# Kernel tuning notes

Hardware: AMD Instinct MI355X
Metric: run time of the kernel (lower is better)

Reference implementation:

```python
import jax, jax.numpy as jnp
import numpy as np

N_T, N_M, E, Q = 100000, 20000, 600000, 200000
F_IN, D, L = 256, 128, 2


def setup_inputs() -> dict:
    key = jax.random.key(0)
    ks = jax.random.split(key, 20)
    s = 1.0 / np.sqrt(D)
    inp = {
        "x_thesis": jax.random.normal(ks[0], (N_T, F_IN), jnp.float32),
        "mentor_node_id": jnp.arange(N_M, dtype=jnp.int64) if jax.config.jax_enable_x64 else jnp.arange(N_M, dtype=jnp.int32),
        "edge_src": jax.random.randint(ks[1], (E,), 0, N_T),
        "edge_dst": jax.random.randint(ks[2], (E,), 0, N_M),
        "eli_src": jax.random.randint(ks[3], (Q,), 0, N_T),
        "eli_dst": jax.random.randint(ks[4], (Q,), 0, N_M),
        # encoder params
        "thesis_lin_w": jax.random.normal(ks[5], (D, F_IN), jnp.float32) / np.sqrt(F_IN),
        "thesis_lin_b": jnp.zeros((D,), jnp.float32),
        "prof_emb": jax.random.normal(ks[6], (N_M, D), jnp.float32),
        # SAGEConv params per layer, per edge type (sup: thesis->mentor, rev: mentor->thesis)
        "W_nbr_sup": jax.random.normal(ks[7], (L, D, D), jnp.float32) * s,
        "W_root_sup": jax.random.normal(ks[8], (L, D, D), jnp.float32) * s,
        "b_sup": jnp.zeros((L, D), jnp.float32),
        "W_nbr_rev": jax.random.normal(ks[9], (L, D, D), jnp.float32) * s,
        "W_root_rev": jax.random.normal(ks[10], (L, D, D), jnp.float32) * s,
        "b_rev": jnp.zeros((L, D), jnp.float32),
        # classifier Linear(2*D -> 1)
        "cls_w": jax.random.normal(ks[11], (2 * D,), jnp.float32) * (1.0 / np.sqrt(2 * D)),
        "cls_b": jnp.zeros((), jnp.float32),
    }
    return inp


def reference(x_thesis, mentor_node_id, edge_src, edge_dst, eli_src, eli_dst,
              thesis_lin_w, thesis_lin_b, prof_emb,
              W_nbr_sup, W_root_sup, b_sup, W_nbr_rev, W_root_rev, b_rev,
              cls_w, cls_b):
    n_t = x_thesis.shape[0]
    n_m = prof_emb.shape[0]
    L_ = W_nbr_sup.shape[0]

    # node encoders
    h_t = x_thesis @ thesis_lin_w.T + thesis_lin_b          # [N_T, D]
    h_m = prof_emb[mentor_node_id]                          # [N_M, D]

    ones = jnp.ones(edge_src.shape[0], h_t.dtype)
    deg_m = jnp.maximum(jax.ops.segment_sum(ones, edge_dst, num_segments=n_m), 1.0)[:, None]
    deg_t = jnp.maximum(jax.ops.segment_sum(ones, edge_src, num_segments=n_t), 1.0)[:, None]

    for l in range(L_):
        # mean-aggregate thesis feats onto mentors (supervised_by edges)
        agg_m = jax.ops.segment_sum(h_t[edge_src], edge_dst, num_segments=n_m) / deg_m
        # mean-aggregate mentor feats onto theses (reverse edges)
        agg_t = jax.ops.segment_sum(h_m[edge_dst], edge_src, num_segments=n_t) / deg_t
        new_m = agg_m @ W_nbr_sup[l].T + h_m @ W_root_sup[l].T + b_sup[l]
        new_t = agg_t @ W_nbr_rev[l].T + h_t @ W_root_rev[l].T + b_rev[l]
        if l < L_ - 1:
            new_m = jax.nn.relu(new_m)
            new_t = jax.nn.relu(new_t)
        h_t, h_m = new_t, new_m

    # edge-level classifier: gather endpoints, concat, linear -> scalar per pair
    z = jnp.concatenate([h_t[eli_src], h_m[eli_dst]], axis=-1)  # [Q, 2D]
    return z @ cls_w + cls_b                                     # [Q]
```

## Files before the change

### kernel.cpp

```cpp
#include <hip/hip_runtime.h>
#include <cstdint>
#include <cstddef>

#define D 128
#define F_IN 256

typedef __attribute__((ext_vector_type(8))) short bf16x8;
typedef __attribute__((ext_vector_type(4))) float f32x4;

__device__ __forceinline__ unsigned short f2bs(float f) {
  unsigned int x = __builtin_bit_cast(unsigned int, f);
  x = x + 0x7fffu + ((x >> 16) & 1u);
  return (unsigned short)(x >> 16);
}
__device__ __forceinline__ unsigned pk2(float lo, float hi) {
  return (unsigned)f2bs(lo) | ((unsigned)f2bs(hi) << 16);
}
__device__ __forceinline__ float b2f(unsigned int lo16) {
  unsigned int x = lo16 << 16;
  return __builtin_bit_cast(float, x);
}
__device__ __forceinline__ void gl_lds16v(const void* g, void* l) {
  __builtin_amdgcn_global_load_lds(
      (__attribute__((address_space(1))) void*)g,
      (__attribute__((address_space(3))) void*)l, 16, 0, 0);
}
__device__ __forceinline__ uint4 pack8(float4 a, float4 b) {
  uint4 o;
  o.x = pk2(a.x, a.y); o.y = pk2(a.z, a.w);
  o.z = pk2(b.x, b.y); o.w = pk2(b.z, b.w);
  return o;
}


__global__ __launch_bounds__(256) void prep_k(
    const float* __restrict__ s0, unsigned short* __restrict__ d0, int n0,
    const float* __restrict__ s1, unsigned short* __restrict__ d1, int n1,
    const float* __restrict__ s2, unsigned short* __restrict__ d2, int n2,
    const float* __restrict__ s3, unsigned short* __restrict__ d3, int n3,
    const float* __restrict__ s4, unsigned short* __restrict__ d4, int n4,
    int nbC,
    const float* __restrict__ emb, const int* __restrict__ ids,
    unsigned short* __restrict__ hm, int NM, int nbG,
    const int* __restrict__ esrc, const int* __restrict__ edst,
    int* __restrict__ bktT, int* __restrict__ bktM,
    int E, int SHT, int SHM, int nbA)
{
  int bid = blockIdx.x;
  int tid = threadIdx.x;
  if (bid < nbC) {
    int j = bid * 256 + tid;
    const float* s; unsigned short* d;
    if (j < n0) { s = s0; d = d0; }
    else {
      j -= n0;
      if (j < n1) { s = s1; d = d1; }
      else {
        j -= n1;
        if (j < n2) { s = s2; d = d2; }
        else {
          j -= n2;
          if (j < n3) { s = s3; d = d3; }
          else { j -= n3; if (j >= n4) return; s = s4; d = d4; }
        }
      }
    }
    const float4* sp = (const float4*)(s + (size_t)j * 8);
    *(uint4*)(d + (size_t)j * 8) = pack8(sp[0], sp[1]);
    return;
  }
  bid -= nbC;
  if (bid < nbG) {
    int i = bid * 256 + tid;
    if (i >= NM * 16) return;
    int r = i >> 4, c = (i & 15) * 8;
    const float* s = emb + (size_t)ids[r] * D + c;
    *(uint4*)(hm + (size_t)r * D + c) = pack8(*(const float4*)s, *(const float4*)(s + 4));
    return;
  }
  bid -= nbG;
  __shared__ int sh[256];
  sh[tid] = 0;
  __syncthreads();
  int stride = nbA * 256;
  for (int e = bid * 256 + tid; e < E; e += stride) {
    atomicAdd(&sh[esrc[e] >> SHT], 1);
    atomicAdd(&sh[128 + (edst[e] >> SHM)], 1);
  }
  __syncthreads();
  if (tid < 128) { if (sh[tid]) atomicAdd(&bktT[tid], sh[tid]); }
  else { if (sh[tid]) atomicAdd(&bktM[tid - 128], sh[tid]); }
}


__global__ void a2_scan_k(const int* __restrict__ bktT, int* __restrict__ baseT, int* __restrict__ curT, int BT,
                          const int* __restrict__ bktM, int* __restrict__ baseM, int* __restrict__ curM, int BM) {
  __shared__ int sT[129], sM[129];
  int tid = threadIdx.x;
  if (tid < BT) sT[tid] = bktT[tid];
  if (tid < BM) sM[tid] = bktM[tid];
  __syncthreads();
  if (tid == 0) { int r = 0; for (int i = 0; i < BT; ++i) { int c = sT[i]; sT[i] = r; r += c; } sT[BT] = r; }
  if (tid == 1) { int r = 0; for (int i = 0; i < BM; ++i) { int c = sM[i]; sM[i] = r; r += c; } sM[BM] = r; }
  __syncthreads();
  if (tid <= BT) { baseT[tid] = sT[tid]; if (tid < BT) curT[tid] = sT[tid]; }
  if (tid <= BM) { baseM[tid] = sM[tid]; if (tid < BM) curM[tid] = sM[tid]; }
}


#define CH 4096

__device__ __forceinline__ void a3_body(
    const int* __restrict__ esrc, const int* __restrict__ edst,
    unsigned* __restrict__ partT, unsigned* __restrict__ partM,
    int* __restrict__ curT, int* __restrict__ curM,
    int E, int BT, int BM, int SHT, int SHM, int blk, char* smraw)
{
  unsigned* stT = (unsigned*)smraw;
  unsigned* stM = stT + CH;
  int* hT  = (int*)(stM + CH);
  int* lbT = hT + 128;
  int* lcT = hT + 256;
  int* gbT = hT + 384;
  int* hM  = hT + 512;
  int* lbM = hT + 640;
  int* lcM = hT + 768;
  int* gbM = hT + 896;
  int* st2 = hT + 1024;

  int tid = threadIdx.x;
  int c0 = blk * CH;
  int len = E - c0; if (len > CH) len = CH;

  if (tid < 128) { hT[tid] = 0; hM[tid] = 0; }
  __syncthreads();
  for (int i = tid; i < len; i += 256) {
    atomicAdd(&hT[esrc[c0 + i] >> SHT], 1);
    atomicAdd(&hM[edst[c0 + i] >> SHM], 1);
  }
  __syncthreads();
  int own = (tid < 128) ? hT[tid] : hM[tid - 128];
  st2[tid] = own;
  __syncthreads();
  for (int dd = 1; dd < 128; dd <<= 1) {
    int y = ((tid & 127) >= dd) ? st2[tid - dd] : 0;
    __syncthreads();
    st2[tid] += y;
    __syncthreads();
  }
  int excl = st2[tid] - own;
  if (tid < 128) { lbT[tid] = excl; lcT[tid] = excl; }
  else { lbM[tid - 128] = excl; lcM[tid - 128] = excl; }
  __syncthreads();
  if (tid < BT) { if (hT[tid]) gbT[tid] = atomicAdd(&curT[tid], hT[tid]); }
  if (tid >= 128 && tid - 128 < BM) { int m = tid - 128; if (hM[m]) gbM[m] = atomicAdd(&curM[m], hM[m]); }
  __syncthreads();
  for (int i = tid; i < len; i += 256) {
    unsigned s = (unsigned)esrc[c0 + i], dn = (unsigned)edst[c0 + i];
    int p = atomicAdd(&lcT[s >> SHT], 1);
    stT[p] = (s << 15) | dn;
    int q = atomicAdd(&lcM[dn >> SHM], 1);
    stM[q] = (dn << 17) | s;
  }
  __syncthreads();
  for (int b = 0; b < BT; ++b) {
    int cb = hT[b]; if (!cb) continue;
    int lb = lbT[b]; int gb = gbT[b];
    for (int i = tid; i < cb; i += 256) partT[gb + i] = stT[lb + i];
  }
  for (int b = 0; b < BM; ++b) {
    int cb = hM[b]; if (!cb) continue;
    int lb = lbM[b]; int gb = gbM[b];
    for (int i = tid; i < cb; i += 256) partM[gb + i] = stM[lb + i];
  }
}


__device__ __forceinline__ void enc_body(
    const float* __restrict__ A, const unsigned short* __restrict__ W,
    const float* __restrict__ bias, unsigned short* __restrict__ out, int M,
    int blk, char* smraw)
{
  float* bufA0 = (float*)smraw;
  unsigned short* bufW0 = (unsigned short*)(smraw + 32768);
  const int tid = threadIdx.x;
  const int w = tid >> 6, l = tid & 63;
  const int wr = w >> 1, wc = w & 1;
  const int lr = l & 15, kg = l >> 4;
  const int row0 = blk * 128;
  const int arow = l >> 3;
  const int au = l & 7;
  const int wrow = l >> 2;
  const int wu = l & 3;

  f32x4 acc[4][4] = {};

  auto stage = [&](int st, int bsel) {
    int k0 = st * 32;
    float* bA = bufA0 + bsel * 4096;
    unsigned short* bW = bufW0 + bsel * 4096;
#pragma unroll
    for (int q = 0; q < 4; ++q) {
      int r = w * 32 + q * 8 + arow;
      int gr = row0 + r; if (gr >= M) gr = M - 1;
      int gu = au ^ (r & 7);
      gl_lds16v(A + (size_t)gr * F_IN + k0 + gu * 4, bA + (w * 32 + q * 8) * 32 + l * 4);
    }
#pragma unroll
    for (int q = 0; q < 2; ++q) {
      int r = w * 32 + q * 16 + wrow;
      int gu = wu ^ ((r >> 1) & 3);
      gl_lds16v(W + (size_t)r * F_IN + k0 + gu * 8, bW + (w * 32 + q * 16) * 32 + l * 8);
    }
  };

  stage(0, 0);
#pragma unroll 1
  for (int st = 0; st < F_IN / 32; ++st) {
    if (st < F_IN / 32 - 1) {
      stage(st + 1, (st + 1) & 1);
      __builtin_amdgcn_sched_barrier(0);
      asm volatile("s_waitcnt vmcnt(6)" ::: "memory");
    } else {
      __builtin_amdgcn_sched_barrier(0);
      asm volatile("s_waitcnt vmcnt(0)" ::: "memory");
    }
    __builtin_amdgcn_s_barrier();
    __builtin_amdgcn_sched_barrier(0);
    const float* bA = bufA0 + (st & 1) * 4096;
    const unsigned short* bW = bufW0 + (st & 1) * 4096;
    bf16x8 aF[4], bF[4];
#pragma unroll
    for (int i = 0; i < 4; ++i) {
      int r = wr * 64 + i * 16 + lr;
      const float4* pa = (const float4*)(bA + r * 32);
      float4 v0 = pa[(2 * kg) ^ (r & 7)];
      float4 v1 = pa[(2 * kg + 1) ^ (r & 7)];
      uint4 c = pack8(v0, v1);
      aF[i] = *(bf16x8*)&c;
    }
#pragma unroll
    for (int j = 0; j < 4; ++j) {
      int r = wc * 64 + j * 16 + lr;
      bF[j] = *(const bf16x8*)&bW[r * 32 + ((kg ^ ((r >> 1) & 3)) * 8)];
    }
#pragma unroll
    for (int i = 0; i < 4; ++i)
#pragma unroll
      for (int j = 0; j < 4; ++j)
        acc[i][j] = __builtin_amdgcn_mfma_f32_16x16x32_bf16(aF[i], bF[j], acc[i][j], 0, 0, 0);
    __builtin_amdgcn_sched_barrier(0);
    __builtin_amdgcn_s_barrier();
  }

  __syncthreads();
  float bn[4];
#pragma unroll
  for (int j = 0; j < 4; ++j) bn[j] = bias[wc * 64 + j * 16 + lr];
  unsigned short* ow = (unsigned short*)smraw + w * 4096;
#pragma unroll
  for (int i = 0; i < 4; ++i)
#pragma unroll
    for (int j = 0; j < 4; ++j) {
      f32x4 v = acc[i][j];
#pragma unroll
      for (int r = 0; r < 4; ++r)
        ow[(i * 16 + kg * 4 + r) * 64 + j * 16 + lr] = f2bs(v[r] + bn[j]);
    }
  __syncthreads();
#pragma unroll
  for (int q = 0; q < 8; ++q) {
    int u = q * 64 + l;
    int lrow = u >> 3;
    int cu = (u & 7) * 8;
    int gr = row0 + wr * 64 + lrow;
    if (gr < M)
      *(uint4*)(out + (size_t)gr * D + wc * 64 + cu) = *(const uint4*)&ow[lrow * 64 + cu];
  }
}

__global__ __launch_bounds__(256) void a3enc_k(
    const int* __restrict__ esrc, const int* __restrict__ edst,
    unsigned* __restrict__ partT, unsigned* __restrict__ partM,
    int* __restrict__ curT, int* __restrict__ curM,
    int E, int BT, int BM, int SHT, int SHM, int nbA3,
    const float* __restrict__ A, const unsigned short* __restrict__ W,
    const float* __restrict__ bias, unsigned short* __restrict__ out, int M)
{
  __shared__ char smraw[49152];
  if ((int)blockIdx.x < nbA3)
    a3_body(esrc, edst, partT, partM, curT, curM, E, BT, BM, SHT, SHM, blockIdx.x, smraw);
  else
    enc_body(A, W, bias, out, M, blockIdx.x - nbA3, smraw);
}


#define BCAP 12288

__global__ __launch_bounds__(256) void b_csr_k(
    const unsigned* __restrict__ partT, const int* __restrict__ baseT,
    int* __restrict__ rowT, int* __restrict__ csrT, int NT, int BT, int SHT,
    const unsigned* __restrict__ partM, const int* __restrict__ baseM,
    int* __restrict__ rowM, int* __restrict__ csrM, int NM, int BM, int SHM, int E)
{
  __shared__ int cnt[1024];
  __shared__ int st[256];
  __shared__ unsigned stage[BCAP];

  const unsigned* part; const int* base; int* row; int* csr;
  int N, SH, KS; unsigned PM; int b; bool last;
  if ((int)blockIdx.x < BT) {
    part = partT; base = baseT; row = rowT; csr = csrT;
    N = NT; SH = SHT; KS = 15; PM = 0x7fffu; b = blockIdx.x; last = (b == BT - 1);
  } else {
    part = partM; base = baseM; row = rowM; csr = csrM;
    N = NM; SH = SHM; KS = 17; PM = 0x1ffffu; b = blockIdx.x - BT; last = (b == BM - 1);
  }
  int tid = threadIdx.x;
  int ebeg = base[b], eend = base[b + 1];
  int tot = eend - ebeg;
  int n0 = b << SH;
  int width = 1 << SH;
  int nw = N - n0; if (nw > width) nw = width;
  int seg = (width + 255) >> 8;

  for (int j = 0; j < seg; ++j) { int idx = tid * seg + j; if (idx < nw) cnt[idx] = 0; }
  __syncthreads();
  for (int i = tid; i < tot; i += 256) {
    int k = (int)(part[ebeg + i] >> KS) - n0;
    atomicAdd(&cnt[k], 1);
  }
  __syncthreads();
  int s = 0;
  for (int j = 0; j < seg; ++j) { int idx = tid * seg + j; if (idx < nw) s += cnt[idx]; }
  st[tid] = s;
  __syncthreads();
  for (int dd = 1; dd < 256; dd <<= 1) {
    int y = (tid >= dd) ? st[tid - dd] : 0;
    __syncthreads();
    st[tid] += y;
    __syncthreads();
  }
  int run = st[tid] - s;
  for (int j = 0; j < seg; ++j) {
    int idx = tid * seg + j;
    if (idx < nw) {
      int c = cnt[idx];
      row[n0 + idx] = ebeg + run;
      cnt[idx] = run;
      run += c;
    }
  }
  if (last && tid == 0) row[N] = E;
  __syncthreads();
  if (tot <= BCAP) {
    for (int i = tid; i < tot; i += 256) {
      unsigned p = part[ebeg + i];
      int k = (int)(p >> KS) - n0;
      int pos = atomicAdd(&cnt[k], 1);
      stage[pos] = p & PM;
    }
    __syncthreads();
    for (int i = tid; i < tot; i += 256) csr[ebeg + i] = (int)stage[i];
  } else {
    for (int i = tid; i < tot; i += 256) {
      unsigned p = part[ebeg + i];
      int k = (int)(p >> KS) - n0;
      int pos = atomicAdd(&cnt[k], 1);
      csr[ebeg + pos] = (int)(p & PM);
    }
  }
}


__global__ __launch_bounds__(256) void aggregate3_k(
    const unsigned short* __restrict__ tabM, const int* __restrict__ rowpM,
    const int* __restrict__ idxM, unsigned short* __restrict__ outM, int nM, int nblkM,
    const unsigned short* __restrict__ tabT, const int* __restrict__ rowpT,
    const int* __restrict__ idxT, unsigned short* __restrict__ outT, int nT)
{
  const unsigned short* tab; const int* rowp; const int* idx;
  unsigned short* outp; int n, nodeb;
  if ((int)blockIdx.x < nblkM) {
    tab = tabM; rowp = rowpM; idx = idxM; outp = outM; n = nM;
    nodeb = blockIdx.x * 8;
  } else {
    tab = tabT; rowp = rowpT; idx = idxT; outp = outT; n = nT;
    nodeb = (blockIdx.x - nblkM) * 8;
  }
  const int tid = threadIdx.x;
  const int l = tid & 63;
  const int sub = l >> 5;
  const int half = (l >> 4) & 1;
  const int l16 = l & 15;
  const int node = nodeb + (tid >> 6) * 2 + sub;
  const int nodeC = node < n ? node : n - 1;
  int b = rowp[nodeC];
  int e = rowp[nodeC + 1];
  if (node >= n) e = b;
  const int deg = e - b;
  int nb = (deg + 15) >> 4;
  int onb = __shfl_xor(nb, 32, 64);
  int trip = nb > onb ? nb : onb;
  const unsigned short* tl = tab + l16 * 8;

  float a0 = 0.f, a1 = 0.f, a2 = 0.f, a3 = 0.f;
  float a4 = 0.f, a5 = 0.f, a6 = 0.f, a7 = 0.f;
  for (int t = 0; t < trip; ++t) {
    int base = b + t * 16 + half;
    int pp[8]; bool ok[8];
#pragma unroll
    for (int u = 0; u < 8; ++u) {
      int p = base + 2 * u;
      ok[u] = p < e;
      pp[u] = ok[u] ? idx[p] : 0;
    }
    uint4 vv[8];
#pragma unroll
    for (int u = 0; u < 8; ++u) {
      uint4 z; z.x = 0u; z.y = 0u; z.z = 0u; z.w = 0u;
      vv[u] = z;
      if (ok[u]) vv[u] = *(const uint4*)(tl + (size_t)pp[u] * D);
    }
#pragma unroll
    for (int u = 0; u < 8; ++u) {
      a0 += b2f(vv[u].x & 0xffffu); a1 += b2f(vv[u].x >> 16);
      a2 += b2f(vv[u].y & 0xffffu); a3 += b2f(vv[u].y >> 16);
      a4 += b2f(vv[u].z & 0xffffu); a5 += b2f(vv[u].z >> 16);
      a6 += b2f(vv[u].w & 0xffffu); a7 += b2f(vv[u].w >> 16);
    }
  }
  a0 += __shfl_xor(a0, 16, 64);
  a1 += __shfl_xor(a1, 16, 64);
  a2 += __shfl_xor(a2, 16, 64);
  a3 += __shfl_xor(a3, 16, 64);
  a4 += __shfl_xor(a4, 16, 64);
  a5 += __shfl_xor(a5, 16, 64);
  a6 += __shfl_xor(a6, 16, 64);
  a7 += __shfl_xor(a7, 16, 64);
  if (node < n && half == 0) {
    float inv = 1.0f / (float)(deg > 1 ? deg : 1);
    uint4 o;
    o.x = pk2(a0 * inv, a1 * inv);
    o.y = pk2(a2 * inv, a3 * inv);
    o.z = pk2(a4 * inv, a5 * inv);
    o.w = pk2(a6 * inv, a7 * inv);
    *(uint4*)(outp + (size_t)node * D + l16 * 8) = o;
  }
}


template<bool RELU>
__device__ __forceinline__ void gemm_body(
    const unsigned short* __restrict__ Aop, const unsigned short* __restrict__ WA,
    const unsigned short* __restrict__ Bop, const unsigned short* __restrict__ WB,
    const float* __restrict__ bias, unsigned short* __restrict__ out, int M,
    int blk, char* smraw)
{
  unsigned short* bufA0 = (unsigned short*)smraw;
  unsigned short* bufW0 = (unsigned short*)(smraw + 16384);
  const int tid = threadIdx.x;
  const int w = tid >> 6, l = tid & 63;
  const int wr = w >> 1, wc = w & 1;
  const int lr = l & 15, kg = l >> 4;
  const int row0 = blk * 128;
  const int srow = l >> 2;
  const int su = l & 3;

  f32x4 acc[4][4] = {};

  auto stage = [&](int st, int bsel) {
    const unsigned short* Ap = (st < 4) ? Aop : Bop;
    const unsigned short* Wp = (st < 4) ? WA : WB;
    int k0 = (st & 3) * 32;
    unsigned short* bA = bufA0 + bsel * 4096;
    unsigned short* bW = bufW0 + bsel * 4096;
#pragma unroll
    for (int q = 0; q < 2; ++q) {
      int r = w * 32 + q * 16 + srow;
      int gr = row0 + r; if (gr >= M) gr = M - 1;
      int gu = su ^ ((r >> 1) & 3);
      gl_lds16v(Ap + (size_t)gr * D + k0 + gu * 8, bA + (w * 32 + q * 16) * 32 + l * 8);
      gl_lds16v(Wp + (size_t)r * D + k0 + gu * 8, bW + (w * 32 + q * 16) * 32 + l * 8);
    }
  };

  stage(0, 0);
#pragma unroll 1
  for (int st = 0; st < 8; ++st) {
    if (st < 7) {
      stage(st + 1, (st + 1) & 1);
      __builtin_amdgcn_sched_barrier(0);
      asm volatile("s_waitcnt vmcnt(4)" ::: "memory");
    } else {
      __builtin_amdgcn_sched_barrier(0);
      asm volatile("s_waitcnt vmcnt(0)" ::: "memory");
    }
    __builtin_amdgcn_s_barrier();
    __builtin_amdgcn_sched_barrier(0);
    const unsigned short* bA = bufA0 + (st & 1) * 4096;
    const unsigned short* bW = bufW0 + (st & 1) * 4096;
    bf16x8 aF[4], bF[4];
#pragma unroll
    for (int i = 0; i < 4; ++i) {
      int r = wr * 64 + i * 16 + lr;
      aF[i] = *(const bf16x8*)&bA[r * 32 + ((kg ^ ((r >> 1) & 3)) * 8)];
    }
#pragma unroll
    for (int j = 0; j < 4; ++j) {
      int r = wc * 64 + j * 16 + lr;
      bF[j] = *(const bf16x8*)&bW[r * 32 + ((kg ^ ((r >> 1) & 3)) * 8)];
    }
#pragma unroll
    for (int i = 0; i < 4; ++i)
#pragma unroll
      for (int j = 0; j < 4; ++j)
        acc[i][j] = __builtin_amdgcn_mfma_f32_16x16x32_bf16(aF[i], bF[j], acc[i][j], 0, 0, 0);
    __builtin_amdgcn_sched_barrier(0);
    __builtin_amdgcn_s_barrier();
  }

  __syncthreads();
  float bn[4];
#pragma unroll
  for (int j = 0; j < 4; ++j) bn[j] = bias[wc * 64 + j * 16 + lr];
  unsigned short* ow = (unsigned short*)smraw + w * 4096;
#pragma unroll
  for (int i = 0; i < 4; ++i)
#pragma unroll
    for (int j = 0; j < 4; ++j) {
      f32x4 v = acc[i][j];
#pragma unroll
      for (int r = 0; r < 4; ++r) {
        float x = v[r] + bn[j];
        if (RELU) x = fmaxf(x, 0.f);
        ow[(i * 16 + kg * 4 + r) * 64 + j * 16 + lr] = f2bs(x);
      }
    }
  __syncthreads();
#pragma unroll
  for (int q = 0; q < 8; ++q) {
    int u = q * 64 + l;
    int lrow = u >> 3;
    int cu = (u & 7) * 8;
    int gr = row0 + wr * 64 + lrow;
    if (gr < M)
      *(uint4*)(out + (size_t)gr * D + wc * 64 + cu) = *(const uint4*)&ow[lrow * 64 + cu];
  }
}

template<bool RELU>
__global__ __launch_bounds__(256) void gemm_pair_k(
    const unsigned short* __restrict__ Am, const unsigned short* __restrict__ WAm,
    const unsigned short* __restrict__ Bm, const unsigned short* __restrict__ WBm,
    const float* __restrict__ biasm, unsigned short* __restrict__ outm, int Mm, int nbm,
    const unsigned short* __restrict__ At, const unsigned short* __restrict__ WAt,
    const unsigned short* __restrict__ Bt, const unsigned short* __restrict__ WBt,
    const float* __restrict__ biast, unsigned short* __restrict__ outt, int Mt)
{
  __shared__ char smraw[32768];
  if ((int)blockIdx.x < nbm)
    gemm_body<RELU>(Am, WAm, Bm, WBm, biasm, outm, Mm, blockIdx.x, smraw);
  else
    gemm_body<RELU>(At, WAt, Bt, WBt, biast, outt, Mt, blockIdx.x - nbm, smraw);
}


__global__ __launch_bounds__(256) void classify_k(
    const unsigned short* __restrict__ ht, const unsigned short* __restrict__ hm,
    const int* __restrict__ qs, const int* __restrict__ qd,
    const float* __restrict__ w, const float* __restrict__ bptr,
    float* __restrict__ out, int Q)
{
  int g = blockIdx.x * 8 + (threadIdx.x >> 5);
  if (g >= Q) return;
  int l = threadIdx.x & 31;
  const unsigned short* src = (l < 16)
      ? ht + (size_t)qs[g] * D + l * 8
      : hm + (size_t)qd[g] * D + (l - 16) * 8;
  uint4 v = *(const uint4*)src;
  const float* wp = w + l * 8;
  float acc = 0.f;
  acc += b2f(v.x & 0xffffu) * wp[0];
  acc += b2f(v.x >> 16)     * wp[1];
  acc += b2f(v.y & 0xffffu) * wp[2];
  acc += b2f(v.y >> 16)     * wp[3];
  acc += b2f(v.z & 0xffffu) * wp[4];
  acc += b2f(v.z >> 16)     * wp[5];
  acc += b2f(v.w & 0xffffu) * wp[6];
  acc += b2f(v.w >> 16)     * wp[7];
#pragma unroll
  for (int m = 16; m >= 1; m >>= 1) acc += __shfl_xor(acc, m, 64);
  if (l == 0) out[g] = acc + bptr[0];
}


extern "C" void kernel_launch(void* const* d_in, const int* in_sizes, int n_in,
                              void* d_out, int out_size, void* d_ws, size_t ws_size,
                              hipStream_t stream)
{
  const float* x_thesis = (const float*)d_in[0];
  const int*   mentor_id = (const int*)d_in[1];
  const int*   esrc = (const int*)d_in[2];
  const int*   edst = (const int*)d_in[3];
  const int*   qsrc = (const int*)d_in[4];
  const int*   qdst = (const int*)d_in[5];
  const float* lin_w = (const float*)d_in[6];
  const float* lin_b = (const float*)d_in[7];
  const float* prof  = (const float*)d_in[8];
  const float* Wn_sup = (const float*)d_in[9];
  const float* Wr_sup = (const float*)d_in[10];
  const float* b_sup  = (const float*)d_in[11];
  const float* Wn_rev = (const float*)d_in[12];
  const float* Wr_rev = (const float*)d_in[13];
  const float* b_rev  = (const float*)d_in[14];
  const float* cls_w  = (const float*)d_in[15];
  const float* cls_b  = (const float*)d_in[16];

  const int NT = in_sizes[0] / F_IN;
  const int NM = in_sizes[1];
  const int E  = in_sizes[2];
  const int Q  = in_sizes[4];
  const int L  = in_sizes[11] / D;

  int SHT = 0; while ((((NT - 1) >> SHT) + 1) > 128) ++SHT;
  int SHM = 0; while ((((NM - 1) >> SHM) + 1) > 128) ++SHM;
  const int BT = ((NT - 1) >> SHT) + 1;
  const int BM = ((NM - 1) >> SHM) + 1;

  char* wsb = (char*)d_ws;
  size_t off = 0;
  auto alloc = [&](size_t bytes) {
    void* p = wsb + off;
    off = (off + bytes + 255) & ~(size_t)255;
    return p;
  };
  unsigned short* h_t   = (unsigned short*)alloc((size_t)NT * D * 2);
  unsigned short* a_t   = (unsigned short*)alloc((size_t)NT * D * 2);
  unsigned short* h_m   = (unsigned short*)alloc((size_t)NM * D * 2);
  unsigned short* a_m   = (unsigned short*)alloc((size_t)NM * D * 2);
  unsigned short* linw_bf = (unsigned short*)alloc((size_t)D * F_IN * 2);
  unsigned short* wns_bf  = (unsigned short*)alloc((size_t)L * D * D * 2);
  unsigned short* wrs_bf  = (unsigned short*)alloc((size_t)L * D * D * 2);
  unsigned short* wnr_bf  = (unsigned short*)alloc((size_t)L * D * D * 2);
  unsigned short* wrr_bf  = (unsigned short*)alloc((size_t)L * D * D * 2);
  int* row_t = (int*)alloc(((size_t)NT + 1) * 4);
  int* row_m = (int*)alloc(((size_t)NM + 1) * 4);
  int* csr_t = (int*)alloc((size_t)E * 4);
  int* csr_m = (int*)alloc((size_t)E * 4);
  unsigned* partT = (unsigned*)alloc((size_t)E * 4);
  unsigned* partM = (unsigned*)alloc((size_t)E * 4);
  size_t bkt_off = off;
  int* bktT  = (int*)alloc(128 * 4);
  int* bktM  = (int*)alloc(128 * 4);
  size_t bkt_end = off;
  int* baseT = (int*)alloc(129 * 4);
  int* baseM = (int*)alloc(129 * 4);
  int* curT  = (int*)alloc(128 * 4);
  int* curM  = (int*)alloc(128 * 4);
  (void)n_in; (void)out_size; (void)ws_size;

  (void)hipMemsetAsync(wsb + bkt_off, 0, bkt_end - bkt_off, stream);

  {
    int n0 = D * F_IN / 8, nw = L * D * D / 8;
    int totc = n0 + 4 * nw;
    int nbC = (totc + 255) / 256;
    int nbG = (NM * 16 + 255) / 256;
    int nbA = 256;
    prep_k<<<nbC + nbG + nbA, 256, 0, stream>>>(
        lin_w, linw_bf, n0, Wn_sup, wns_bf, nw, Wr_sup, wrs_bf, nw,
        Wn_rev, wnr_bf, nw, Wr_rev, wrr_bf, nw, nbC,
        prof, mentor_id, h_m, NM, nbG,
        esrc, edst, bktT, bktM, E, SHT, SHM, nbA);
  }
  a2_scan_k<<<1, 256, 0, stream>>>(bktT, baseT, curT, BT, bktM, baseM, curM, BM);

  int nbA3 = (E + CH - 1) / CH;
  int nbEnc = (NT + 127) / 128;
  a3enc_k<<<nbA3 + nbEnc, 256, 0, stream>>>(
      esrc, edst, partT, partM, curT, curM, E, BT, BM, SHT, SHM, nbA3,
      x_thesis, linw_bf, lin_b, h_t, NT);

  b_csr_k<<<BT + BM, 256, 0, stream>>>(
      partT, baseT, row_t, csr_t, NT, BT, SHT,
      partM, baseM, row_m, csr_m, NM, BM, SHM, E);

  int agg_nbm = (NM + 7) / 8, agg_nbt = (NT + 7) / 8;
  int gem_nbm = (NM + 127) / 128, gem_nbt = (NT + 127) / 128;
  for (int l = 0; l < L; ++l) {
    aggregate3_k<<<agg_nbm + agg_nbt, 256, 0, stream>>>(
        h_t, row_m, csr_m, a_m, NM, agg_nbm,
        h_m, row_t, csr_t, a_t, NT);

    const unsigned short* wns = wns_bf + (size_t)l * D * D;
    const unsigned short* wrs = wrs_bf + (size_t)l * D * D;
    const unsigned short* wnr = wnr_bf + (size_t)l * D * D;
    const unsigned short* wrr = wrr_bf + (size_t)l * D * D;
    const float* bs = b_sup + (size_t)l * D;
    const float* br = b_rev + (size_t)l * D;
    if (l < L - 1) {
      gemm_pair_k<true><<<gem_nbm + gem_nbt, 256, 0, stream>>>(
          a_m, wns, h_m, wrs, bs, a_m, NM, gem_nbm,
          a_t, wnr, h_t, wrr, br, a_t, NT);
    } else {
      gemm_pair_k<false><<<gem_nbm + gem_nbt, 256, 0, stream>>>(
          a_m, wns, h_m, wrs, bs, a_m, NM, gem_nbm,
          a_t, wnr, h_t, wrr, br, a_t, NT);
    }
    unsigned short* tmp;
    tmp = h_t; h_t = a_t; a_t = tmp;
    tmp = h_m; h_m = a_m; a_m = tmp;
  }

  classify_k<<<(Q + 7) / 8, 256, 0, stream>>>(h_t, h_m, qsrc, qdst, cls_w, cls_b,
                                              (float*)d_out, Q);
}
```

Before: 256.8 us.

## Move thesis encoder into prep kernel with in-register fp32-to-bf16 conversion

The thesis encoder GEMM moves from the partition kernel into the prep kernel. It now reads fp32 x and the fp32 linear weight directly, converting to bf16 in registers, so the separate weight-conversion pass and the linw_bf buffer are gone. A-operand loads go through registers with software prefetch instead of global-to-LDS async copies, which cuts LDS use to 32KB. The partition step becomes its own smaller kernel. This reshapes which work overlaps with what: the encoder now runs alongside the bucket counting instead of the partition, and the global-to-LDS async copy path for A is dropped.

```diff
diff --git a/kernel.cpp b/kernel.cpp
--- a/kernel.cpp
+++ b/kernel.cpp
@@ -33,8 +33,115 @@
 }
 
 
-__global__ __launch_bounds__(256) void prep_k(
-    const float* __restrict__ s0, unsigned short* __restrict__ d0, int n0,
+__device__ __forceinline__ void enc_body(
+    const float* __restrict__ A, const float* __restrict__ Wf,
+    const float* __restrict__ bias, unsigned short* __restrict__ out, int M,
+    int blk, char* smraw)
+{
+  unsigned short* bufW0 = (unsigned short*)smraw;
+  const int tid = threadIdx.x;
+  const int w = tid >> 6, l = tid & 63;
+  const int wr = w >> 1, wc = w & 1;
+  const int lr = l & 15, kg = l >> 4;
+  const int row0 = blk * 128;
+
+  const float* ap[4];
+#pragma unroll
+  for (int i = 0; i < 4; ++i) {
+    int gr = row0 + wr * 64 + i * 16 + lr;
+    if (gr >= M) gr = M - 1;
+    ap[i] = A + (size_t)gr * F_IN + kg * 8;
+  }
+  const int wrow = tid >> 1, wh = tid & 1;
+  const float* wsrc = Wf + (size_t)wrow * F_IN + wh * 16;
+  const int wswz = (wrow >> 1) & 3;
+
+  f32x4 acc[4][4] = {};
+  float4 aCur[8], aNxt[8];
+#pragma unroll
+  for (int i = 0; i < 4; ++i) {
+    aCur[2 * i]     = *(const float4*)(ap[i]);
+    aCur[2 * i + 1] = *(const float4*)(ap[i] + 4);
+  }
+  {
+    const float4* s4 = (const float4*)wsrc;
+    float4 w0 = s4[0], w1 = s4[1], w2 = s4[2], w3 = s4[3];
+    unsigned short* bW = bufW0 + wrow * 32;
+    *(uint4*)(bW + ((2 * wh) ^ wswz) * 8)     = pack8(w0, w1);
+    *(uint4*)(bW + ((2 * wh + 1) ^ wswz) * 8) = pack8(w2, w3);
+  }
+  __syncthreads();
+
+#pragma unroll 1
+  for (int st = 0; st < F_IN / 32; ++st) {
+    const unsigned short* bW = bufW0 + (st & 1) * 4096;
+    bf16x8 wF[4];
+#pragma unroll
+    for (int j = 0; j < 4; ++j) {
+      int r = wc * 64 + j * 16 + lr;
+      wF[j] = *(const bf16x8*)&bW[r * 32 + ((kg ^ ((r >> 1) & 3)) * 8)];
+    }
+    if (st < F_IN / 32 - 1) {
+      const float4* s4 = (const float4*)(wsrc + (st + 1) * 32);
+      float4 w0 = s4[0], w1 = s4[1], w2 = s4[2], w3 = s4[3];
+      unsigned short* bWn = bufW0 + ((st + 1) & 1) * 4096 + wrow * 32;
+      *(uint4*)(bWn + ((2 * wh) ^ wswz) * 8)     = pack8(w0, w1);
+      *(uint4*)(bWn + ((2 * wh + 1) ^ wswz) * 8) = pack8(w2, w3);
+#pragma unroll
+      for (int i = 0; i < 4; ++i) {
+        aNxt[2 * i]     = *(const float4*)(ap[i] + (st + 1) * 32);
+        aNxt[2 * i + 1] = *(const float4*)(ap[i] + (st + 1) * 32 + 4);
+      }
+    }
+    bf16x8 aF[4];
+#pragma unroll
+    for (int i = 0; i < 4; ++i) {
+      uint4 c = pack8(aCur[2 * i], aCur[2 * i + 1]);
+      aF[i] = *(bf16x8*)&c;
+    }
+#pragma unroll
+    for (int i = 0; i < 4; ++i)
+#pragma unroll
+      for (int j = 0; j < 4; ++j)
+        acc[i][j] = __builtin_amdgcn_mfma_f32_16x16x32_bf16(aF[i], wF[j], acc[i][j], 0, 0, 0);
+    if (st < F_IN / 32 - 1) {
+#pragma unroll
+      for (int i = 0; i < 8; ++i) aCur[i] = aNxt[i];
+    }
+    asm volatile("s_waitcnt lgkmcnt(0)" ::: "memory");
+    __builtin_amdgcn_sched_barrier(0);
+    __builtin_amdgcn_s_barrier();
+    __builtin_amdgcn_sched_barrier(0);
+  }
+
+  __syncthreads();
+  float bn[4];
+#pragma unroll
+  for (int j = 0; j < 4; ++j) bn[j] = bias[wc * 64 + j * 16 + lr];
+  unsigned short* ow = (unsigned short*)smraw + w * 4096;
+#pragma unroll
+  for (int i = 0; i < 4; ++i)
+#pragma unroll
+    for (int j = 0; j < 4; ++j) {
+      f32x4 v = acc[i][j];
+#pragma unroll
+      for (int r = 0; r < 4; ++r)
+        ow[(i * 16 + kg * 4 + r) * 64 + j * 16 + lr] = f2bs(v[r] + bn[j]);
+    }
+  __syncthreads();
+#pragma unroll
+  for (int q = 0; q < 8; ++q) {
+    int u = q * 64 + l;
+    int lrow = u >> 3;
+    int cu = (u & 7) * 8;
+    int gr = row0 + wr * 64 + lrow;
+    if (gr < M)
+      *(uint4*)(out + (size_t)gr * D + wc * 64 + cu) = *(const uint4*)&ow[lrow * 64 + cu];
+  }
+}
+
+
+__global__ __launch_bounds__(256) void prepenc_k(
     const float* __restrict__ s1, unsigned short* __restrict__ d1, int n1,
     const float* __restrict__ s2, unsigned short* __restrict__ d2, int n2,
     const float* __restrict__ s3, unsigned short* __restrict__ d3, int n3,
@@ -44,25 +151,24 @@
     unsigned short* __restrict__ hm, int NM, int nbG,
     const int* __restrict__ esrc, const int* __restrict__ edst,
     int* __restrict__ bktT, int* __restrict__ bktM,
-    int E, int SHT, int SHM, int nbA)
-{
+    int E, int SHT, int SHM, int nbA,
+    const float* __restrict__ xA, const float* __restrict__ Wf,
+    const float* __restrict__ bias, unsigned short* __restrict__ ht, int M)
+{
+  __shared__ char smraw[32768];
   int bid = blockIdx.x;
   int tid = threadIdx.x;
   if (bid < nbC) {
     int j = bid * 256 + tid;
     const float* s; unsigned short* d;
-    if (j < n0) { s = s0; d = d0; }
+    if (j < n1) { s = s1; d = d1; }
     else {
-      j -= n0;
-      if (j < n1) { s = s1; d = d1; }
+      j -= n1;
+      if (j < n2) { s = s2; d = d2; }
       else {
-        j -= n1;
-        if (j < n2) { s = s2; d = d2; }
-        else {
-          j -= n2;
-          if (j < n3) { s = s3; d = d3; }
-          else { j -= n3; if (j >= n4) return; s = s4; d = d4; }
-        }
+        j -= n2;
+        if (j < n3) { s = s3; d = d3; }
+        else { j -= n3; if (j >= n4) return; s = s4; d = d4; }
       }
     }
     const float4* sp = (const float4*)(s + (size_t)j * 8);
@@ -79,17 +185,22 @@
     return;
   }
   bid -= nbG;
-  __shared__ int sh[256];
-  sh[tid] = 0;
-  __syncthreads();
-  int stride = nbA * 256;
-  for (int e = bid * 256 + tid; e < E; e += stride) {
-    atomicAdd(&sh[esrc[e] >> SHT], 1);
-    atomicAdd(&sh[128 + (edst[e] >> SHM)], 1);
-  }
-  __syncthreads();
-  if (tid < 128) { if (sh[tid]) atomicAdd(&bktT[tid], sh[tid]); }
-  else { if (sh[tid]) atomicAdd(&bktM[tid - 128], sh[tid]); }
+  if (bid < nbA) {
+    int* sh = (int*)smraw;
+    sh[tid] = 0;
+    __syncthreads();
+    int stride = nbA * 256;
+    for (int e = bid * 256 + tid; e < E; e += stride) {
+      atomicAdd(&sh[esrc[e] >> SHT], 1);
+      atomicAdd(&sh[128 + (edst[e] >> SHM)], 1);
+    }
+    __syncthreads();
+    if (tid < 128) { if (sh[tid]) atomicAdd(&bktT[tid], sh[tid]); }
+    else { if (sh[tid]) atomicAdd(&bktM[tid - 128], sh[tid]); }
+    return;
+  }
+  bid -= nbA;
+  enc_body(xA, Wf, bias, ht, M, bid, smraw);
 }
 
 
@@ -110,26 +221,18 @@
 
 #define CH 4096
 
-__device__ __forceinline__ void a3_body(
+__global__ __launch_bounds__(256) void a3_part_k(
     const int* __restrict__ esrc, const int* __restrict__ edst,
     unsigned* __restrict__ partT, unsigned* __restrict__ partM,
     int* __restrict__ curT, int* __restrict__ curM,
-    int E, int BT, int BM, int SHT, int SHM, int blk, char* smraw)
-{
-  unsigned* stT = (unsigned*)smraw;
-  unsigned* stM = stT + CH;
-  int* hT  = (int*)(stM + CH);
-  int* lbT = hT + 128;
-  int* lcT = hT + 256;
-  int* gbT = hT + 384;
-  int* hM  = hT + 512;
-  int* lbM = hT + 640;
-  int* lcM = hT + 768;
-  int* gbM = hT + 896;
-  int* st2 = hT + 1024;
-
+    int E, int BT, int BM, int SHT, int SHM)
+{
+  __shared__ unsigned stT[CH], stM[CH];
+  __shared__ int hT[128], lbT[128], lcT[128], gbT[128];
+  __shared__ int hM[128], lbM[128], lcM[128], gbM[128];
+  __shared__ int st2[256];
   int tid = threadIdx.x;
-  int c0 = blk * CH;
+  int c0 = blockIdx.x * CH;
   int len = E - c0; if (len > CH) len = CH;
 
   if (tid < 128) { hT[tid] = 0; hM[tid] = 0; }
@@ -173,125 +276,6 @@
     int lb = lbM[b]; int gb = gbM[b];
     for (int i = tid; i < cb; i += 256) partM[gb + i] = stM[lb + i];
   }
-}
-
-
-__device__ __forceinline__ void enc_body(
-    const float* __restrict__ A, const unsigned short* __restrict__ W,
-    const float* __restrict__ bias, unsigned short* __restrict__ out, int M,
-    int blk, char* smraw)
-{
-  float* bufA0 = (float*)smraw;
-  unsigned short* bufW0 = (unsigned short*)(smraw + 32768);
-  const int tid = threadIdx.x;
-  const int w = tid >> 6, l = tid & 63;
-  const int wr = w >> 1, wc = w & 1;
-  const int lr = l & 15, kg = l >> 4;
-  const int row0 = blk * 128;
-  const int arow = l >> 3;
-  const int au = l & 7;
-  const int wrow = l >> 2;
-  const int wu = l & 3;
-
-  f32x4 acc[4][4] = {};
-
-  auto stage = [&](int st, int bsel) {
-    int k0 = st * 32;
-    float* bA = bufA0 + bsel * 4096;
-    unsigned short* bW = bufW0 + bsel * 4096;
-#pragma unroll
-    for (int q = 0; q < 4; ++q) {
-      int r = w * 32 + q * 8 + arow;
-      int gr = row0 + r; if (gr >= M) gr = M - 1;
-      int gu = au ^ (r & 7);
-      gl_lds16v(A + (size_t)gr * F_IN + k0 + gu * 4, bA + (w * 32 + q * 8) * 32 + l * 4);
-    }
-#pragma unroll
-    for (int q = 0; q < 2; ++q) {
-      int r = w * 32 + q * 16 + wrow;
-      int gu = wu ^ ((r >> 1) & 3);
-      gl_lds16v(W + (size_t)r * F_IN + k0 + gu * 8, bW + (w * 32 + q * 16) * 32 + l * 8);
-    }
-  };
-
-  stage(0, 0);
-#pragma unroll 1
-  for (int st = 0; st < F_IN / 32; ++st) {
-    if (st < F_IN / 32 - 1) {
-      stage(st + 1, (st + 1) & 1);
-      __builtin_amdgcn_sched_barrier(0);
-      asm volatile("s_waitcnt vmcnt(6)" ::: "memory");
-    } else {
-      __builtin_amdgcn_sched_barrier(0);
-      asm volatile("s_waitcnt vmcnt(0)" ::: "memory");
-    }
-    __builtin_amdgcn_s_barrier();
-    __builtin_amdgcn_sched_barrier(0);
-    const float* bA = bufA0 + (st & 1) * 4096;
-    const unsigned short* bW = bufW0 + (st & 1) * 4096;
-    bf16x8 aF[4], bF[4];
-#pragma unroll
-    for (int i = 0; i < 4; ++i) {
-      int r = wr * 64 + i * 16 + lr;
-      const float4* pa = (const float4*)(bA + r * 32);
-      float4 v0 = pa[(2 * kg) ^ (r & 7)];
-      float4 v1 = pa[(2 * kg + 1) ^ (r & 7)];
-      uint4 c = pack8(v0, v1);
-      aF[i] = *(bf16x8*)&c;
-    }
-#pragma unroll
-    for (int j = 0; j < 4; ++j) {
-      int r = wc * 64 + j * 16 + lr;
-      bF[j] = *(const bf16x8*)&bW[r * 32 + ((kg ^ ((r >> 1) & 3)) * 8)];
-    }
-#pragma unroll
-    for (int i = 0; i < 4; ++i)
-#pragma unroll
-      for (int j = 0; j < 4; ++j)
-        acc[i][j] = __builtin_amdgcn_mfma_f32_16x16x32_bf16(aF[i], bF[j], acc[i][j], 0, 0, 0);
-    __builtin_amdgcn_sched_barrier(0);
-    __builtin_amdgcn_s_barrier();
-  }
-
-  __syncthreads();
-  float bn[4];
-#pragma unroll
-  for (int j = 0; j < 4; ++j) bn[j] = bias[wc * 64 + j * 16 + lr];
-  unsigned short* ow = (unsigned short*)smraw + w * 4096;
-#pragma unroll
-  for (int i = 0; i < 4; ++i)
-#pragma unroll
-    for (int j = 0; j < 4; ++j) {
-      f32x4 v = acc[i][j];
-#pragma unroll
-      for (int r = 0; r < 4; ++r)
-        ow[(i * 16 + kg * 4 + r) * 64 + j * 16 + lr] = f2bs(v[r] + bn[j]);
-    }
-  __syncthreads();
-#pragma unroll
-  for (int q = 0; q < 8; ++q) {
-    int u = q * 64 + l;
-    int lrow = u >> 3;
-    int cu = (u & 7) * 8;
-    int gr = row0 + wr * 64 + lrow;
-    if (gr < M)
-      *(uint4*)(out + (size_t)gr * D + wc * 64 + cu) = *(const uint4*)&ow[lrow * 64 + cu];
-  }
-}
-
-__global__ __launch_bounds__(256) void a3enc_k(
-    const int* __restrict__ esrc, const int* __restrict__ edst,
-    unsigned* __restrict__ partT, unsigned* __restrict__ partM,
-    int* __restrict__ curT, int* __restrict__ curM,
-    int E, int BT, int BM, int SHT, int SHM, int nbA3,
-    const float* __restrict__ A, const unsigned short* __restrict__ W,
-    const float* __restrict__ bias, unsigned short* __restrict__ out, int M)
-{
-  __shared__ char smraw[49152];
-  if ((int)blockIdx.x < nbA3)
-    a3_body(esrc, edst, partT, partM, curT, curM, E, BT, BM, SHT, SHM, blockIdx.x, smraw);
-  else
-    enc_body(A, W, bias, out, M, blockIdx.x - nbA3, smraw);
 }
 
 
@@ -639,7 +623,6 @@
   unsigned short* a_t   = (unsigned short*)alloc((size_t)NT * D * 2);
   unsigned short* h_m   = (unsigned short*)alloc((size_t)NM * D * 2);
   unsigned short* a_m   = (unsigned short*)alloc((size_t)NM * D * 2);
-  unsigned short* linw_bf = (unsigned short*)alloc((size_t)D * F_IN * 2);
   unsigned short* wns_bf  = (unsigned short*)alloc((size_t)L * D * D * 2);
   unsigned short* wrs_bf  = (unsigned short*)alloc((size_t)L * D * D * 2);
   unsigned short* wnr_bf  = (unsigned short*)alloc((size_t)L * D * D * 2);
@@ -663,25 +646,22 @@
   (void)hipMemsetAsync(wsb + bkt_off, 0, bkt_end - bkt_off, stream);
 
   {
-    int n0 = D * F_IN / 8, nw = L * D * D / 8;
-    int totc = n0 + 4 * nw;
+    int nw = L * D * D / 8;
+    int totc = 4 * nw;
     int nbC = (totc + 255) / 256;
     int nbG = (NM * 16 + 255) / 256;
     int nbA = 256;
-    prep_k<<<nbC + nbG + nbA, 256, 0, stream>>>(
-        lin_w, linw_bf, n0, Wn_sup, wns_bf, nw, Wr_sup, wrs_bf, nw,
+    int nbEnc = (NT + 127) / 128;
+    prepenc_k<<<nbC + nbG + nbA + nbEnc, 256, 0, stream>>>(
+        Wn_sup, wns_bf, nw, Wr_sup, wrs_bf, nw,
         Wn_rev, wnr_bf, nw, Wr_rev, wrr_bf, nw, nbC,
         prof, mentor_id, h_m, NM, nbG,
-        esrc, edst, bktT, bktM, E, SHT, SHM, nbA);
+        esrc, edst, bktT, bktM, E, SHT, SHM, nbA,
+        x_thesis, lin_w, lin_b, h_t, NT);
   }
   a2_scan_k<<<1, 256, 0, stream>>>(bktT, baseT, curT, BT, bktM, baseM, curM, BM);
-
-  int nbA3 = (E + CH - 1) / CH;
-  int nbEnc = (NT + 127) / 128;
-  a3enc_k<<<nbA3 + nbEnc, 256, 0, stream>>>(
-      esrc, edst, partT, partM, curT, curM, E, BT, BM, SHT, SHM, nbA3,
-      x_thesis, linw_bf, lin_b, h_t, NT);
-
+  a3_part_k<<<(E + CH - 1) / CH, 256, 0, stream>>>(
+      esrc, edst, partT, partM, curT, curM, E, BT, BM, SHT, SHM);
   b_csr_k<<<BT + BM, 256, 0, stream>>>(
       partT, baseT, row_t, csr_t, NT, BT, SHT,
       partM, baseM, row_m, csr_m, NM, BM, SHM, E);
```

Result: slower. 281.9 us (+9.7%).

## Split fused partition/encoder kernel and single-buffer encoder GEMM to cut LDS

Applied to the files above, without the earlier changes.

Separates the edge-partition pass and the thesis encoder GEMM into their own kernels instead of one fused launch sharing a 48KB LDS block. The new encoder uses a single 24KB LDS buffer with plain syncthreads, dropping the double-buffered prefetch, and writes its output through a half-block staging pass. The aim is higher occupancy for both stages, since neither has to reserve LDS for the other anymore. The cost is losing load/compute overlap within the GEMM and the concurrency between partitioning and encoding; the encoder now also runs after the CSR build.

```diff
diff --git a/kernel.cpp b/kernel.cpp
--- a/kernel.cpp
+++ b/kernel.cpp
@@ -110,26 +110,18 @@
 
 #define CH 4096
 
-__device__ __forceinline__ void a3_body(
+__global__ __launch_bounds__(256) void a3_part_k(
     const int* __restrict__ esrc, const int* __restrict__ edst,
     unsigned* __restrict__ partT, unsigned* __restrict__ partM,
     int* __restrict__ curT, int* __restrict__ curM,
-    int E, int BT, int BM, int SHT, int SHM, int blk, char* smraw)
-{
-  unsigned* stT = (unsigned*)smraw;
-  unsigned* stM = stT + CH;
-  int* hT  = (int*)(stM + CH);
-  int* lbT = hT + 128;
-  int* lcT = hT + 256;
-  int* gbT = hT + 384;
-  int* hM  = hT + 512;
-  int* lbM = hT + 640;
-  int* lcM = hT + 768;
-  int* gbM = hT + 896;
-  int* st2 = hT + 1024;
-
+    int E, int BT, int BM, int SHT, int SHM)
+{
+  __shared__ unsigned stT[CH], stM[CH];
+  __shared__ int hT[128], lbT[128], lcT[128], gbT[128];
+  __shared__ int hM[128], lbM[128], lcM[128], gbM[128];
+  __shared__ int st2[256];
   int tid = threadIdx.x;
-  int c0 = blk * CH;
+  int c0 = blockIdx.x * CH;
   int len = E - c0; if (len > CH) len = CH;
 
   if (tid < 128) { hT[tid] = 0; hM[tid] = 0; }
@@ -173,125 +165,6 @@
     int lb = lbM[b]; int gb = gbM[b];
     for (int i = tid; i < cb; i += 256) partM[gb + i] = stM[lb + i];
   }
-}
-
-
-__device__ __forceinline__ void enc_body(
-    const float* __restrict__ A, const unsigned short* __restrict__ W,
-    const float* __restrict__ bias, unsigned short* __restrict__ out, int M,
-    int blk, char* smraw)
-{
-  float* bufA0 = (float*)smraw;
-  unsigned short* bufW0 = (unsigned short*)(smraw + 32768);
-  const int tid = threadIdx.x;
-  const int w = tid >> 6, l = tid & 63;
-  const int wr = w >> 1, wc = w & 1;
-  const int lr = l & 15, kg = l >> 4;
-  const int row0 = blk * 128;
-  const int arow = l >> 3;
-  const int au = l & 7;
-  const int wrow = l >> 2;
-  const int wu = l & 3;
-
-  f32x4 acc[4][4] = {};
-
-  auto stage = [&](int st, int bsel) {
-    int k0 = st * 32;
-    float* bA = bufA0 + bsel * 4096;
-    unsigned short* bW = bufW0 + bsel * 4096;
-#pragma unroll
-    for (int q = 0; q < 4; ++q) {
-      int r = w * 32 + q * 8 + arow;
-      int gr = row0 + r; if (gr >= M) gr = M - 1;
-      int gu = au ^ (r & 7);
-      gl_lds16v(A + (size_t)gr * F_IN + k0 + gu * 4, bA + (w * 32 + q * 8) * 32 + l * 4);
-    }
-#pragma unroll
-    for (int q = 0; q < 2; ++q) {
-      int r = w * 32 + q * 16 + wrow;
-      int gu = wu ^ ((r >> 1) & 3);
-      gl_lds16v(W + (size_t)r * F_IN + k0 + gu * 8, bW + (w * 32 + q * 16) * 32 + l * 8);
-    }
-  };
-
-  stage(0, 0);
-#pragma unroll 1
-  for (int st = 0; st < F_IN / 32; ++st) {
-    if (st < F_IN / 32 - 1) {
-      stage(st + 1, (st + 1) & 1);
-      __builtin_amdgcn_sched_barrier(0);
-      asm volatile("s_waitcnt vmcnt(6)" ::: "memory");
-    } else {
-      __builtin_amdgcn_sched_barrier(0);
-      asm volatile("s_waitcnt vmcnt(0)" ::: "memory");
-    }
-    __builtin_amdgcn_s_barrier();
-    __builtin_amdgcn_sched_barrier(0);
-    const float* bA = bufA0 + (st & 1) * 4096;
-    const unsigned short* bW = bufW0 + (st & 1) * 4096;
-    bf16x8 aF[4], bF[4];
-#pragma unroll
-    for (int i = 0; i < 4; ++i) {
-      int r = wr * 64 + i * 16 + lr;
-      const float4* pa = (const float4*)(bA + r * 32);
-      float4 v0 = pa[(2 * kg) ^ (r & 7)];
-      float4 v1 = pa[(2 * kg + 1) ^ (r & 7)];
-      uint4 c = pack8(v0, v1);
-      aF[i] = *(bf16x8*)&c;
-    }
-#pragma unroll
-    for (int j = 0; j < 4; ++j) {
-      int r = wc * 64 + j * 16 + lr;
-      bF[j] = *(const bf16x8*)&bW[r * 32 + ((kg ^ ((r >> 1) & 3)) * 8)];
-    }
-#pragma unroll
-    for (int i = 0; i < 4; ++i)
-#pragma unroll
-      for (int j = 0; j < 4; ++j)
-        acc[i][j] = __builtin_amdgcn_mfma_f32_16x16x32_bf16(aF[i], bF[j], acc[i][j], 0, 0, 0);
-    __builtin_amdgcn_sched_barrier(0);
-    __builtin_amdgcn_s_barrier();
-  }
-
-  __syncthreads();
-  float bn[4];
-#pragma unroll
-  for (int j = 0; j < 4; ++j) bn[j] = bias[wc * 64 + j * 16 + lr];
-  unsigned short* ow = (unsigned short*)smraw + w * 4096;
-#pragma unroll
-  for (int i = 0; i < 4; ++i)
-#pragma unroll
-    for (int j = 0; j < 4; ++j) {
-      f32x4 v = acc[i][j];
-#pragma unroll
-      for (int r = 0; r < 4; ++r)
-        ow[(i * 16 + kg * 4 + r) * 64 + j * 16 + lr] = f2bs(v[r] + bn[j]);
-    }
-  __syncthreads();
-#pragma unroll
-  for (int q = 0; q < 8; ++q) {
-    int u = q * 64 + l;
-    int lrow = u >> 3;
-    int cu = (u & 7) * 8;
-    int gr = row0 + wr * 64 + lrow;
-    if (gr < M)
-      *(uint4*)(out + (size_t)gr * D + wc * 64 + cu) = *(const uint4*)&ow[lrow * 64 + cu];
-  }
-}
-
-__global__ __launch_bounds__(256) void a3enc_k(
-    const int* __restrict__ esrc, const int* __restrict__ edst,
-    unsigned* __restrict__ partT, unsigned* __restrict__ partM,
-    int* __restrict__ curT, int* __restrict__ curM,
-    int E, int BT, int BM, int SHT, int SHM, int nbA3,
-    const float* __restrict__ A, const unsigned short* __restrict__ W,
-    const float* __restrict__ bias, unsigned short* __restrict__ out, int M)
-{
-  __shared__ char smraw[49152];
-  if ((int)blockIdx.x < nbA3)
-    a3_body(esrc, edst, partT, partM, curT, curM, E, BT, BM, SHT, SHM, blockIdx.x, smraw);
-  else
-    enc_body(A, W, bias, out, M, blockIdx.x - nbA3, smraw);
 }
 
 
@@ -368,6 +241,95 @@
       int k = (int)(p >> KS) - n0;
       int pos = atomicAdd(&cnt[k], 1);
       csr[ebeg + pos] = (int)(p & PM);
+    }
+  }
+}
+
+
+__global__ __launch_bounds__(256) void enc24_k(
+    const float* __restrict__ A, const unsigned short* __restrict__ W,
+    const float* __restrict__ bias, unsigned short* __restrict__ out, int M)
+{
+  __shared__ char smraw[24576];
+  float* bufA = (float*)smraw;
+  unsigned short* bufW = (unsigned short*)(smraw + 16384);
+  const int tid = threadIdx.x;
+  const int w = tid >> 6, l = tid & 63;
+  const int wr = w >> 1, wc = w & 1;
+  const int lr = l & 15, kg = l >> 4;
+  const int row0 = blockIdx.x * 128;
+  const int arow = l >> 3, au = l & 7;
+  const int wrow = l >> 2, wu = l & 3;
+
+  f32x4 acc[4][4] = {};
+
+#pragma unroll 1
+  for (int st = 0; st < F_IN / 32; ++st) {
+    int k0 = st * 32;
+#pragma unroll
+    for (int q = 0; q < 4; ++q) {
+      int r = w * 32 + q * 8 + arow;
+      int gr = row0 + r; if (gr >= M) gr = M - 1;
+      int gu = au ^ (r & 7);
+      gl_lds16v(A + (size_t)gr * F_IN + k0 + gu * 4, bufA + r * 32 + au * 4);
+    }
+#pragma unroll
+    for (int q = 0; q < 2; ++q) {
+      int r = w * 32 + q * 16 + wrow;
+      int gu = wu ^ ((r >> 1) & 3);
+      gl_lds16v(W + (size_t)r * F_IN + k0 + gu * 8, bufW + r * 32 + wu * 8);
+    }
+    __syncthreads();
+    bf16x8 aF[4], wF[4];
+#pragma unroll
+    for (int i = 0; i < 4; ++i) {
+      int r = wr * 64 + i * 16 + lr;
+      const float4* pa = (const float4*)(bufA + r * 32);
+      float4 v0 = pa[(2 * kg) ^ (r & 7)];
+      float4 v1 = pa[(2 * kg + 1) ^ (r & 7)];
+      uint4 c = pack8(v0, v1);
+      aF[i] = *(bf16x8*)&c;
+    }
+#pragma unroll
+    for (int j = 0; j < 4; ++j) {
+      int r = wc * 64 + j * 16 + lr;
+      wF[j] = *(const bf16x8*)&bufW[r * 32 + ((kg ^ ((r >> 1) & 3)) * 8)];
+    }
+#pragma unroll
+    for (int i = 0; i < 4; ++i)
+#pragma unroll
+      for (int j = 0; j < 4; ++j)
+        acc[i][j] = __builtin_amdgcn_mfma_f32_16x16x32_bf16(aF[i], wF[j], acc[i][j], 0, 0, 0);
+    __syncthreads();
+  }
+
+  float bn[4];
+#pragma unroll
+  for (int j = 0; j < 4; ++j) bn[j] = bias[wc * 64 + j * 16 + lr];
+  unsigned short* stg = (unsigned short*)smraw;
+#pragma unroll 1
+  for (int half = 0; half < 2; ++half) {
+    __syncthreads();
+    if (wr == half) {
+#pragma unroll
+      for (int i = 0; i < 4; ++i)
+#pragma unroll
+        for (int j = 0; j < 4; ++j) {
+          f32x4 v = acc[i][j];
+#pragma unroll
+          for (int r = 0; r < 4; ++r)
+            stg[(i * 16 + kg * 4 + r) * 128 + wc * 64 + j * 16 + lr] = f2bs(v[r] + bn[j]);
+        }
+    }
+    __syncthreads();
+#pragma unroll
+    for (int q = 0; q < 4; ++q) {
+      int u = q * 256 + tid;
+      int lrow = u >> 4;
+      int cu = (u & 15) * 8;
+      int gr = row0 + half * 64 + lrow;
+      if (gr < M)
+        *(uint4*)(out + (size_t)gr * D + cu) = *(const uint4*)&stg[lrow * 128 + cu];
     }
   }
 }
@@ -675,16 +637,13 @@
         esrc, edst, bktT, bktM, E, SHT, SHM, nbA);
   }
   a2_scan_k<<<1, 256, 0, stream>>>(bktT, baseT, curT, BT, bktM, baseM, curM, BM);
-
-  int nbA3 = (E + CH - 1) / CH;
-  int nbEnc = (NT + 127) / 128;
-  a3enc_k<<<nbA3 + nbEnc, 256, 0, stream>>>(
-      esrc, edst, partT, partM, curT, curM, E, BT, BM, SHT, SHM, nbA3,
-      x_thesis, linw_bf, lin_b, h_t, NT);
-
+  a3_part_k<<<(E + CH - 1) / CH, 256, 0, stream>>>(
+      esrc, edst, partT, partM, curT, curM, E, BT, BM, SHT, SHM);
   b_csr_k<<<BT + BM, 256, 0, stream>>>(
       partT, baseT, row_t, csr_t, NT, BT, SHT,
       partM, baseM, row_m, csr_m, NM, BM, SHM, E);
+
+  enc24_k<<<(NT + 127) / 128, 256, 0, stream>>>(x_thesis, linw_bf, lin_b, h_t, NT);
 
   int agg_nbm = (NM + 7) / 8, agg_nbt = (NT + 7) / 8;
   int gem_nbm = (NM + 127) / 128, gem_nbt = (NT + 127) / 128;
```

Result: slower. 271.0 us (+5.5%).
